# Kernel optimization log

Measured on AMD Instinct MI355X. Metric: run time of the kernel, lower is better.

## Reference

```python
import jax, jax.numpy as jnp
import numpy as np
from jax.scipy.special import digamma

K_NEIGHBOURS = 5  # matches init_kwargs nNeighbours


def setup_inputs() -> dict:
    key = jax.random.key(0)
    k1, k2 = jax.random.split(key)
    x = jax.random.normal(k1, (2, 2, 64, 64), dtype=jnp.float32)
    y = jax.random.normal(k2, (2, 2, 64, 64), dtype=jnp.float32)
    return {"x": x, "y": y}


def _knn_mi(x, y, k):
    # KSG k-NN mutual information estimator, channel-wise.
    B, C, H, W = x.shape
    BC, HW = B * C, H * W
    xv = x.reshape(BC, HW)
    yv = y.reshape(BC, HW)
    # Pairwise L1 (scalar -> abs diff) distance matrices: (BC, HW, HW)
    dx = jnp.abs(xv[:, :, None] - xv[:, None, :])
    dy = jnp.abs(yv[:, :, None] - yv[:, None, :])
    # Joint-space Chebyshev distance (max over the two marginals)
    z = jnp.maximum(dx, dy)
    # eps = (k+1)-th smallest joint distance per point (includes self-distance 0),
    # matching torch .topk(k+1, largest=False).values[..., -1:]
    neg_smallest = jax.lax.top_k(-z, k + 1)[0]       # (BC, HW, k+1), descending in -z
    eps = -neg_smallest[:, :, -1:]                    # (BC, HW, 1)
    # Marginal neighbor counts with strict < eps (self included, as in torch code)
    nx = jnp.sum(dx < eps, axis=-1).astype(jnp.float32)  # (BC, HW)
    ny = jnp.sum(dy < eps, axis=-1).astype(jnp.float32)
    const = digamma(jnp.float32(k)) + digamma(jnp.float32(HW))
    mi = const - jnp.mean(digamma(nx) + digamma(ny), axis=-1)  # (BC,)
    return jnp.maximum(mi.reshape(B, C), 0.0)


def reference(x, y):
    return _knn_mi(x, y, K_NEIGHBOURS)
```

## Files before the change

### kernel.cpp

```cpp
#include <hip/hip_runtime.h>
#include <math.h>

#define HW 4096
#define NCH 4
#define TPB 1024
#define ROWS_PER_BLOCK 64
#define BLOCKS_PER_CH 64
#define NBLOCKS (NCH * BLOCKS_PER_CH)
#define KNN 5
#define WINB 704

#define NBINS 512
#define BLO   (-6.0f)
#define BDELTA 0.0234375f
#define BINV  (512.0f / 12.0f)
#define SLOP  1e-5f
#define INFT  3.4e38f

#define WS_BXY   16384
#define WS_BY    32768
#define WS_PREF  49152
#define WS_PART  57344

__device__ __forceinline__ int binOf(float v) {
    int b = (int)floorf((v - BLO) * BINV);
    return min(max(b, 0), NBINS - 1);
}

__device__ __forceinline__ float digammaf_dev(float x) {
    float r = 0.f;
    while (x < 6.f) { r -= 1.f / x; x += 1.f; }
    float f = 1.f / x, f2 = f * f;
    return logf(x) - 0.5f * f
         - f2 * (1.f / 12.f - f2 * (1.f / 120.f - f2 * (1.f / 252.f))) + r;
}

__device__ __forceinline__ void insert6(float (&s)[6], float d) {
    float n0 = fminf(s[0], d);
    float n1 = __builtin_amdgcn_fmed3f(s[0], s[1], d);
    float n2 = __builtin_amdgcn_fmed3f(s[1], s[2], d);
    float n3 = __builtin_amdgcn_fmed3f(s[2], s[3], d);
    float n4 = __builtin_amdgcn_fmed3f(s[3], s[4], d);
    float n5 = __builtin_amdgcn_fmed3f(s[4], s[5], d);
    s[0] = n0; s[1] = n1; s[2] = n2; s[3] = n3; s[4] = n4; s[5] = n5;
}

__global__ __launch_bounds__(256) void knnmi_bucketize(const float* __restrict__ x,
                                                       const float* __restrict__ y,
                                                       float* __restrict__ ws) {
    __shared__ int h[NBINS];
    const int c    = blockIdx.x >> 1;
    const int side = blockIdx.x & 1;
    const int t    = threadIdx.x;
    const float* src  = (side == 0 ? x : y) + c * HW;
    const float* ysrc = y + c * HW;
    int* pref = (int*)ws + WS_PREF + (side ? NCH * (NBINS + 1) : 0) + c * (NBINS + 1);

    for (int i = t; i < NBINS; i += 256) h[i] = 0;
    __syncthreads();

    float vx[16], vy[16];
    int bn[16];
#pragma unroll
    for (int k = 0; k < 16; ++k) {
        int i = t + k * 256;
        float v = src[i];
        vx[k] = v;
        vy[k] = (side == 0) ? ysrc[i] : 0.f;
        bn[k] = binOf(v);
        atomicAdd(&h[bn[k]], 1);
    }
    __syncthreads();

    if (t < 64) {
        int sinc[8];
        sinc[0] = h[t * 8 + 0];
#pragma unroll
        for (int j = 1; j < 8; ++j) sinc[j] = sinc[j - 1] + h[t * 8 + j];
        int tot = sinc[7], inc = tot;
#pragma unroll
        for (int off = 1; off < 64; off <<= 1) {
            int u = __shfl_up(inc, off);
            if (t >= off) inc += u;
        }
        int ex = inc - tot;
#pragma unroll
        for (int j = 0; j < 8; ++j) {
            int st = ex + (j ? sinc[j - 1] : 0);
            h[t * 8 + j]    = st;
            pref[t * 8 + j] = st;
        }
        if (t == 63) pref[NBINS] = HW;
    }
    __syncthreads();

    if (side == 0) {
        float* bxx = ws + c * HW;
        float* bxy = ws + WS_BXY + c * HW;
#pragma unroll
        for (int k = 0; k < 16; ++k) {
            int pos = atomicAdd(&h[bn[k]], 1);
            bxx[pos] = vx[k];
            bxy[pos] = vy[k];
        }
    } else {
        float* by = ws + WS_BY + c * HW;
#pragma unroll
        for (int k = 0; k < 16; ++k) {
            int pos = atomicAdd(&h[bn[k]], 1);
            by[pos] = vx[k];
        }
    }
}

__global__ __launch_bounds__(TPB, 4) void knnmi_rows(float* __restrict__ ws) {
    __shared__ float2 swin[WINB];
    __shared__ int pfy[NBINS + 1];
    __shared__ float red[ROWS_PER_BLOCK];

    const int c  = blockIdx.x >> 6;
    const int rb = blockIdx.x & 63;
    const int R0 = rb * ROWS_PER_BLOCK;
    const float* bxx = ws + c * HW;
    const float* bxy = ws + WS_BXY + c * HW;
    const float* by  = ws + WS_BY  + c * HW;
    const int* prefy = (const int*)ws + WS_PREF + NCH * (NBINS + 1) + c * (NBINS + 1);

    int LO = R0 - 320;
    LO = max(LO, 0); LO = min(LO, HW - WINB); LO &= ~3;
    const int HI = LO + WINB;

    const float xLm1 = (LO > 0)  ? bxx[LO - 1] : 0.f;
    const float xHIv = (HI < HW) ? bxx[HI]     : 0.f;

    if (threadIdx.x < WINB / 4) {
        float4 xv = ((const float4*)(bxx + LO))[threadIdx.x];
        float4 yv = ((const float4*)(bxy + LO))[threadIdx.x];
        ((float4*)swin)[2 * threadIdx.x]     = make_float4(xv.x, yv.x, xv.y, yv.y);
        ((float4*)swin)[2 * threadIdx.x + 1] = make_float4(xv.z, yv.z, xv.w, yv.w);
    }
    if (threadIdx.x <= NBINS) pfy[threadIdx.x] = prefy[threadIdx.x];
    __syncthreads();

    const int wv   = threadIdx.x >> 6;
    const int lane = threadIdx.x & 63;
    const int l    = lane & 15;
    const int g    = lane >> 4;
    const int q    = wv * 4 + g;
    const int p    = R0 + q;

    const float xi = swin[p - LO].x;
    const float yi = swin[p - LO].y;

    float s[6];
#pragma unroll
    for (int k = 0; k < 6; ++k) s[k] = INFT;

    const float4* f4 = (const float4*)swin;
#pragma unroll 4
    for (int it = 0; it < WINB / 32; ++it) {
        float4 pp = f4[it * 16 + l];
        insert6(s, fmaxf(fabsf(xi - pp.x), fabsf(yi - pp.y)));
        insert6(s, fmaxf(fabsf(xi - pp.z), fabsf(yi - pp.w)));
    }

#pragma unroll
    for (int m = 1; m < 16; m <<= 1) {
        float o[6];
#pragma unroll
        for (int k = 0; k < 6; ++k) o[k] = __shfl_xor(s[k], m);
#pragma unroll
        for (int k = 0; k < 6; ++k) insert6(s, o[k]);
    }
    float eps = s[5];

    float eL = INFT, eR = INFT;
    if (LO > 0) {
        int b = binOf(xLm1);
        eL = xi - (BLO + (float)(b + 1) * BDELTA + SLOP);
    }
    if (HI < HW) {
        int b = binOf(xHIv);
        eR = (BLO + (float)b * BDELTA - SLOP) - xi;
    }
    const bool ok = (eps <= eL) && (eps <= eR);

    int nx = 0, ny = 0;
    bool fell = false;
    unsigned long long bad = __ballot((l == 0) && !ok);
    while (bad) {
        int bit = (int)__ffsll(bad) - 1;
        bad &= bad - 1;
        const int tg = bit >> 4;
        const float xt = swin[(R0 + wv * 4 + tg) - LO].x;
        const float yt = swin[(R0 + wv * 4 + tg) - LO].y;
        float s3[6];
#pragma unroll
        for (int k = 0; k < 6; ++k) s3[k] = INFT;
        for (int it = 0; it < HW / 256; ++it) {
            float4 xv = ((const float4*)bxx)[it * 64 + lane];
            float4 yv = ((const float4*)bxy)[it * 64 + lane];
            insert6(s3, fmaxf(fabsf(xt - xv.x), fabsf(yt - yv.x)));
            insert6(s3, fmaxf(fabsf(xt - xv.y), fabsf(yt - yv.y)));
            insert6(s3, fmaxf(fabsf(xt - xv.z), fabsf(yt - yv.z)));
            insert6(s3, fmaxf(fabsf(xt - xv.w), fabsf(yt - yv.w)));
        }
#pragma unroll
        for (int m = 1; m < 64; m <<= 1) {
            float o[6];
#pragma unroll
            for (int k = 0; k < 6; ++k) o[k] = __shfl_xor(s3[k], m);
#pragma unroll
            for (int k = 0; k < 6; ++k) insert6(s3, o[k]);
        }
        const float e3 = s3[5];
        int cx = 0, cy = 0;
        for (int it = 0; it < HW / 256; ++it) {
            float4 xv = ((const float4*)bxx)[it * 64 + lane];
            float4 yv = ((const float4*)bxy)[it * 64 + lane];
            cx += (fabsf(xt - xv.x) < e3) + (fabsf(xt - xv.y) < e3)
                + (fabsf(xt - xv.z) < e3) + (fabsf(xt - xv.w) < e3);
            cy += (fabsf(yt - yv.x) < e3) + (fabsf(yt - yv.y) < e3)
                + (fabsf(yt - yv.z) < e3) + (fabsf(yt - yv.w) < e3);
        }
        int pk3 = (cx << 16) | cy;
#pragma unroll
        for (int m = 1; m < 64; m <<= 1) pk3 += __shfl_xor(pk3, m);
        if (g == tg) { eps = e3; nx = pk3 >> 16; ny = pk3 & 0xffff; fell = true; }
    }

    if (!fell) {
#pragma unroll 4
        for (int it = 0; it < WINB / 32; ++it) {
            float4 pp = f4[it * 16 + l];
            nx += (fabsf(xi - pp.x) < eps) + (fabsf(xi - pp.z) < eps);
        }
        int loB = binOf(yi - eps), hiB = binOf(yi + eps);
        int fLo = loB + 2, fHi = hiB - 2;
        if (fLo <= fHi) {
            if (l == 0) ny += pfy[fHi + 1] - pfy[fLo];
            int a0 = pfy[max(loB - 1, 0)], a1 = pfy[min(loB + 1, NBINS - 1) + 1];
            int b0 = pfy[max(hiB - 1, 0)], b1 = pfy[min(hiB + 1, NBINS - 1) + 1];
            for (int tt = a0 + l; tt < a1; tt += 16) ny += (fabsf(by[tt] - yi) < eps);
            for (int tt = b0 + l; tt < b1; tt += 16) ny += (fabsf(by[tt] - yi) < eps);
        } else {
            int a0 = pfy[max(loB - 1, 0)], a1 = pfy[min(hiB + 1, NBINS - 1) + 1];
            for (int tt = a0 + l; tt < a1; tt += 16) ny += (fabsf(by[tt] - yi) < eps);
        }
    }

    if (fell && l != 0) { nx = 0; ny = 0; }
    int pk = (nx << 16) | ny;
#pragma unroll
    for (int m = 1; m < 16; m <<= 1) pk += __shfl_xor(pk, m);

    if (l == 0)
        red[q] = digammaf_dev((float)(pk >> 16)) + digammaf_dev((float)(pk & 0xffff));
    __syncthreads();

    if (threadIdx.x == 0) {
        float v = 0.f;
#pragma unroll
        for (int k = 0; k < ROWS_PER_BLOCK; ++k) v += red[k];
        (ws + WS_PART)[blockIdx.x] = v;
    }
}

__global__ void knnmi_final(const float* __restrict__ ws, float* __restrict__ out) {
    const float* partials = ws + WS_PART;
    const int w    = threadIdx.x >> 6;
    const int lane = threadIdx.x & 63;
    float sum = (lane < BLOCKS_PER_CH) ? partials[w * BLOCKS_PER_CH + lane] : 0.f;
#pragma unroll
    for (int m = 32; m; m >>= 1) sum += __shfl_xor(sum, m);
    if (lane == 0) {
        float mi = digammaf_dev((float)KNN) + digammaf_dev((float)HW)
                 - sum / (float)HW;
        out[w] = fmaxf(mi, 0.f);
    }
}

extern "C" void kernel_launch(void* const* d_in, const int* in_sizes, int n_in,
                              void* d_out, int out_size, void* d_ws, size_t ws_size,
                              hipStream_t stream) {
    const float* x = (const float*)d_in[0];
    const float* y = (const float*)d_in[1];
    float* out = (float*)d_out;
    float* ws  = (float*)d_ws;

    knnmi_bucketize<<<2 * NCH, 256, 0, stream>>>(x, y, ws);
    knnmi_rows<<<NBLOCKS, TPB, 0, stream>>>(ws);
    knnmi_final<<<1, NCH * 64, 0, stream>>>(ws, out);
}
```

Measured before the change: 32.66 us.

## Process rows in four sliding windows per 256-thread block with double-buffered prefetch

```diff
diff --git a/kernel.cpp b/kernel.cpp
--- a/kernel.cpp
+++ b/kernel.cpp
@@ -3,12 +3,13 @@
 
 #define HW 4096
 #define NCH 4
-#define TPB 1024
-#define ROWS_PER_BLOCK 64
+#define TPB 256
+#define WPB 4
+#define ROWS_PER_WINDOW 16
 #define BLOCKS_PER_CH 64
 #define NBLOCKS (NCH * BLOCKS_PER_CH)
 #define KNN 5
-#define WINB 704
+#define WINB 544
 
 #define NBINS 512
 #define BLO   (-6.0f)
@@ -114,156 +115,186 @@
 }
 
 __global__ __launch_bounds__(TPB, 4) void knnmi_rows(float* __restrict__ ws) {
-    __shared__ float2 swin[WINB];
+    __shared__ float2 swin[2][WINB];
     __shared__ int pfy[NBINS + 1];
-    __shared__ float red[ROWS_PER_BLOCK];
+    __shared__ float red[ROWS_PER_WINDOW];
 
     const int c  = blockIdx.x >> 6;
     const int rb = blockIdx.x & 63;
-    const int R0 = rb * ROWS_PER_BLOCK;
     const float* bxx = ws + c * HW;
     const float* bxy = ws + WS_BXY + c * HW;
     const float* by  = ws + WS_BY  + c * HW;
     const int* prefy = (const int*)ws + WS_PREF + NCH * (NBINS + 1) + c * (NBINS + 1);
 
-    int LO = R0 - 320;
-    LO = max(LO, 0); LO = min(LO, HW - WINB); LO &= ~3;
-    const int HI = LO + WINB;
-
-    const float xLm1 = (LO > 0)  ? bxx[LO - 1] : 0.f;
-    const float xHIv = (HI < HW) ? bxx[HI]     : 0.f;
+    for (int i = threadIdx.x; i <= NBINS; i += TPB) pfy[i] = prefy[i];
+
+    int LOg[WPB];
+    float sentL[WPB], sentR[WPB];
+#pragma unroll
+    for (int g = 0; g < WPB; ++g) {
+        int R0 = (rb * WPB + g) * ROWS_PER_WINDOW;
+        int LO = R0 - 264;
+        LO = max(LO, 0); LO = min(LO, HW - WINB); LO &= ~3;
+        LOg[g] = LO;
+        sentL[g] = (LO > 0)         ? bxx[LO - 1]    : 0.f;
+        sentR[g] = (LO + WINB < HW) ? bxx[LO + WINB] : 0.f;
+    }
 
     if (threadIdx.x < WINB / 4) {
-        float4 xv = ((const float4*)(bxx + LO))[threadIdx.x];
-        float4 yv = ((const float4*)(bxy + LO))[threadIdx.x];
-        ((float4*)swin)[2 * threadIdx.x]     = make_float4(xv.x, yv.x, xv.y, yv.y);
-        ((float4*)swin)[2 * threadIdx.x + 1] = make_float4(xv.z, yv.z, xv.w, yv.w);
-    }
-    if (threadIdx.x <= NBINS) pfy[threadIdx.x] = prefy[threadIdx.x];
+        float4 xv = ((const float4*)(bxx + LOg[0]))[threadIdx.x];
+        float4 yv = ((const float4*)(bxy + LOg[0]))[threadIdx.x];
+        ((float4*)swin[0])[2 * threadIdx.x]     = make_float4(xv.x, yv.x, xv.y, yv.y);
+        ((float4*)swin[0])[2 * threadIdx.x + 1] = make_float4(xv.z, yv.z, xv.w, yv.w);
+    }
     __syncthreads();
 
     const int wv   = threadIdx.x >> 6;
     const int lane = threadIdx.x & 63;
     const int l    = lane & 15;
-    const int g    = lane >> 4;
-    const int q    = wv * 4 + g;
-    const int p    = R0 + q;
-
-    const float xi = swin[p - LO].x;
-    const float yi = swin[p - LO].y;
-
-    float s[6];
-#pragma unroll
-    for (int k = 0; k < 6; ++k) s[k] = INFT;
-
-    const float4* f4 = (const float4*)swin;
-#pragma unroll 4
-    for (int it = 0; it < WINB / 32; ++it) {
-        float4 pp = f4[it * 16 + l];
-        insert6(s, fmaxf(fabsf(xi - pp.x), fabsf(yi - pp.y)));
-        insert6(s, fmaxf(fabsf(xi - pp.z), fabsf(yi - pp.w)));
-    }
-
-#pragma unroll
-    for (int m = 1; m < 16; m <<= 1) {
-        float o[6];
-#pragma unroll
-        for (int k = 0; k < 6; ++k) o[k] = __shfl_xor(s[k], m);
-#pragma unroll
-        for (int k = 0; k < 6; ++k) insert6(s, o[k]);
-    }
-    float eps = s[5];
-
-    float eL = INFT, eR = INFT;
-    if (LO > 0) {
-        int b = binOf(xLm1);
-        eL = xi - (BLO + (float)(b + 1) * BDELTA + SLOP);
-    }
-    if (HI < HW) {
-        int b = binOf(xHIv);
-        eR = (BLO + (float)b * BDELTA - SLOP) - xi;
-    }
-    const bool ok = (eps <= eL) && (eps <= eR);
-
-    int nx = 0, ny = 0;
-    bool fell = false;
-    unsigned long long bad = __ballot((l == 0) && !ok);
-    while (bad) {
-        int bit = (int)__ffsll(bad) - 1;
-        bad &= bad - 1;
-        const int tg = bit >> 4;
-        const float xt = swin[(R0 + wv * 4 + tg) - LO].x;
-        const float yt = swin[(R0 + wv * 4 + tg) - LO].y;
-        float s3[6];
-#pragma unroll
-        for (int k = 0; k < 6; ++k) s3[k] = INFT;
-        for (int it = 0; it < HW / 256; ++it) {
-            float4 xv = ((const float4*)bxx)[it * 64 + lane];
-            float4 yv = ((const float4*)bxy)[it * 64 + lane];
-            insert6(s3, fmaxf(fabsf(xt - xv.x), fabsf(yt - yv.x)));
-            insert6(s3, fmaxf(fabsf(xt - xv.y), fabsf(yt - yv.y)));
-            insert6(s3, fmaxf(fabsf(xt - xv.z), fabsf(yt - yv.z)));
-            insert6(s3, fmaxf(fabsf(xt - xv.w), fabsf(yt - yv.w)));
-        }
-#pragma unroll
-        for (int m = 1; m < 64; m <<= 1) {
-            float o[6];
-#pragma unroll
-            for (int k = 0; k < 6; ++k) o[k] = __shfl_xor(s3[k], m);
-#pragma unroll
-            for (int k = 0; k < 6; ++k) insert6(s3, o[k]);
-        }
-        const float e3 = s3[5];
-        int cx = 0, cy = 0;
-        for (int it = 0; it < HW / 256; ++it) {
-            float4 xv = ((const float4*)bxx)[it * 64 + lane];
-            float4 yv = ((const float4*)bxy)[it * 64 + lane];
-            cx += (fabsf(xt - xv.x) < e3) + (fabsf(xt - xv.y) < e3)
-                + (fabsf(xt - xv.z) < e3) + (fabsf(xt - xv.w) < e3);
-            cy += (fabsf(yt - yv.x) < e3) + (fabsf(yt - yv.y) < e3)
-                + (fabsf(yt - yv.z) < e3) + (fabsf(yt - yv.w) < e3);
-        }
-        int pk3 = (cx << 16) | cy;
-#pragma unroll
-        for (int m = 1; m < 64; m <<= 1) pk3 += __shfl_xor(pk3, m);
-        if (g == tg) { eps = e3; nx = pk3 >> 16; ny = pk3 & 0xffff; fell = true; }
-    }
-
-    if (!fell) {
+    const int g16  = lane >> 4;
+    const int q    = wv * 4 + g16;
+
+    float acc = 0.f;
+
+    for (int g = 0; g < WPB; ++g) {
+        float4 pxv, pyv;
+        const bool pf = (g + 1 < WPB) && (threadIdx.x < WINB / 4);
+        if (pf) {
+            pxv = ((const float4*)(bxx + LOg[g + 1]))[threadIdx.x];
+            pyv = ((const float4*)(bxy + LOg[g + 1]))[threadIdx.x];
+        }
+
+        const float2* wbuf = swin[g & 1];
+        const float4* f4   = (const float4*)wbuf;
+        const int LO = LOg[g];
+        const int HI = LO + WINB;
+        const int R0 = (rb * WPB + g) * ROWS_PER_WINDOW;
+        const int p  = R0 + q;
+
+        const float xi = wbuf[p - LO].x;
+        const float yi = wbuf[p - LO].y;
+
+        float s[6];
+#pragma unroll
+        for (int k = 0; k < 6; ++k) s[k] = INFT;
+
 #pragma unroll 4
         for (int it = 0; it < WINB / 32; ++it) {
             float4 pp = f4[it * 16 + l];
-            nx += (fabsf(xi - pp.x) < eps) + (fabsf(xi - pp.z) < eps);
-        }
-        int loB = binOf(yi - eps), hiB = binOf(yi + eps);
-        int fLo = loB + 2, fHi = hiB - 2;
-        if (fLo <= fHi) {
-            if (l == 0) ny += pfy[fHi + 1] - pfy[fLo];
-            int a0 = pfy[max(loB - 1, 0)], a1 = pfy[min(loB + 1, NBINS - 1) + 1];
-            int b0 = pfy[max(hiB - 1, 0)], b1 = pfy[min(hiB + 1, NBINS - 1) + 1];
-            for (int tt = a0 + l; tt < a1; tt += 16) ny += (fabsf(by[tt] - yi) < eps);
-            for (int tt = b0 + l; tt < b1; tt += 16) ny += (fabsf(by[tt] - yi) < eps);
-        } else {
-            int a0 = pfy[max(loB - 1, 0)], a1 = pfy[min(hiB + 1, NBINS - 1) + 1];
-            for (int tt = a0 + l; tt < a1; tt += 16) ny += (fabsf(by[tt] - yi) < eps);
-        }
-    }
-
-    if (fell && l != 0) { nx = 0; ny = 0; }
-    int pk = (nx << 16) | ny;
-#pragma unroll
-    for (int m = 1; m < 16; m <<= 1) pk += __shfl_xor(pk, m);
-
-    if (l == 0)
-        red[q] = digammaf_dev((float)(pk >> 16)) + digammaf_dev((float)(pk & 0xffff));
-    __syncthreads();
-
-    if (threadIdx.x == 0) {
-        float v = 0.f;
-#pragma unroll
-        for (int k = 0; k < ROWS_PER_BLOCK; ++k) v += red[k];
-        (ws + WS_PART)[blockIdx.x] = v;
-    }
+            insert6(s, fmaxf(fabsf(xi - pp.x), fabsf(yi - pp.y)));
+            insert6(s, fmaxf(fabsf(xi - pp.z), fabsf(yi - pp.w)));
+        }
+
+#pragma unroll
+        for (int m = 1; m < 16; m <<= 1) {
+            float o[6];
+#pragma unroll
+            for (int k = 0; k < 6; ++k) o[k] = __shfl_xor(s[k], m);
+#pragma unroll
+            for (int k = 0; k < 6; ++k) insert6(s, o[k]);
+        }
+        float eps = s[5];
+
+        float eL = INFT, eR = INFT;
+        if (LO > 0) {
+            int b = binOf(sentL[g]);
+            eL = xi - (BLO + (float)(b + 1) * BDELTA + SLOP);
+        }
+        if (HI < HW) {
+            int b = binOf(sentR[g]);
+            eR = (BLO + (float)b * BDELTA - SLOP) - xi;
+        }
+        const bool ok = (eps <= eL) && (eps <= eR);
+
+        int nx = 0, ny = 0;
+        bool fell = false;
+        unsigned long long bad = __ballot((l == 0) && !ok);
+        while (bad) {
+            int bit = (int)__ffsll(bad) - 1;
+            bad &= bad - 1;
+            const int tg = bit >> 4;
+            const float xt = wbuf[(R0 + wv * 4 + tg) - LO].x;
+            const float yt = wbuf[(R0 + wv * 4 + tg) - LO].y;
+            float s3[6];
+#pragma unroll
+            for (int k = 0; k < 6; ++k) s3[k] = INFT;
+            for (int it = 0; it < HW / 256; ++it) {
+                float4 xv = ((const float4*)bxx)[it * 64 + lane];
+                float4 yv = ((const float4*)bxy)[it * 64 + lane];
+                insert6(s3, fmaxf(fabsf(xt - xv.x), fabsf(yt - yv.x)));
+                insert6(s3, fmaxf(fabsf(xt - xv.y), fabsf(yt - yv.y)));
+                insert6(s3, fmaxf(fabsf(xt - xv.z), fabsf(yt - yv.z)));
+                insert6(s3, fmaxf(fabsf(xt - xv.w), fabsf(yt - yv.w)));
+            }
+#pragma unroll
+            for (int m = 1; m < 64; m <<= 1) {
+                float o[6];
+#pragma unroll
+                for (int k = 0; k < 6; ++k) o[k] = __shfl_xor(s3[k], m);
+#pragma unroll
+                for (int k = 0; k < 6; ++k) insert6(s3, o[k]);
+            }
+            const float e3 = s3[5];
+            int cx = 0, cy = 0;
+            for (int it = 0; it < HW / 256; ++it) {
+                float4 xv = ((const float4*)bxx)[it * 64 + lane];
+                float4 yv = ((const float4*)bxy)[it * 64 + lane];
+                cx += (fabsf(xt - xv.x) < e3) + (fabsf(xt - xv.y) < e3)
+                    + (fabsf(xt - xv.z) < e3) + (fabsf(xt - xv.w) < e3);
+                cy += (fabsf(yt - yv.x) < e3) + (fabsf(yt - yv.y) < e3)
+                    + (fabsf(yt - yv.z) < e3) + (fabsf(yt - yv.w) < e3);
+            }
+            int pk3 = (cx << 16) | cy;
+#pragma unroll
+            for (int m = 1; m < 64; m <<= 1) pk3 += __shfl_xor(pk3, m);
+            if (g16 == tg) { eps = e3; nx = pk3 >> 16; ny = pk3 & 0xffff; fell = true; }
+        }
+
+        if (!fell) {
+#pragma unroll 4
+            for (int it = 0; it < WINB / 32; ++it) {
+                float4 pp = f4[it * 16 + l];
+                nx += (fabsf(xi - pp.x) < eps) + (fabsf(xi - pp.z) < eps);
+            }
+            int loB = binOf(yi - eps), hiB = binOf(yi + eps);
+            int fLo = loB + 2, fHi = hiB - 2;
+            if (fLo <= fHi) {
+                if (l == 0) ny += pfy[fHi + 1] - pfy[fLo];
+                int a0 = pfy[max(loB - 1, 0)], a1 = pfy[min(loB + 1, NBINS - 1) + 1];
+                int b0 = pfy[max(hiB - 1, 0)], b1 = pfy[min(hiB + 1, NBINS - 1) + 1];
+                for (int tt = a0 + l; tt < a1; tt += 16) ny += (fabsf(by[tt] - yi) < eps);
+                for (int tt = b0 + l; tt < b1; tt += 16) ny += (fabsf(by[tt] - yi) < eps);
+            } else {
+                int a0 = pfy[max(loB - 1, 0)], a1 = pfy[min(hiB + 1, NBINS - 1) + 1];
+                for (int tt = a0 + l; tt < a1; tt += 16) ny += (fabsf(by[tt] - yi) < eps);
+            }
+        }
+
+        if (fell && l != 0) { nx = 0; ny = 0; }
+        int pk = (nx << 16) | ny;
+#pragma unroll
+        for (int m = 1; m < 16; m <<= 1) pk += __shfl_xor(pk, m);
+
+        if (l == 0)
+            red[q] = digammaf_dev((float)(pk >> 16)) + digammaf_dev((float)(pk & 0xffff));
+        __syncthreads();
+
+        if (pf) {
+            ((float4*)swin[(g + 1) & 1])[2 * threadIdx.x]     =
+                make_float4(pxv.x, pyv.x, pxv.y, pyv.y);
+            ((float4*)swin[(g + 1) & 1])[2 * threadIdx.x + 1] =
+                make_float4(pxv.z, pyv.z, pxv.w, pyv.w);
+        }
+        if (threadIdx.x == 0) {
+            float v = 0.f;
+#pragma unroll
+            for (int k = 0; k < ROWS_PER_WINDOW; ++k) v += red[k];
+            acc += v;
+        }
+        __syncthreads();
+    }
+
+    if (threadIdx.x == 0) (ws + WS_PART)[blockIdx.x] = acc;
 }
 
 __global__ void knnmi_final(const float* __restrict__ ws, float* __restrict__ out) {
```

Measured after the change: 53.41 us. 1.64x slower.
